# Kernel optimization log

Measured on AMD Instinct MI355X. Metric: run time of the kernel, lower is better.

## Reference

```python
import jax, jax.numpy as jnp
import numpy as np

N_HEADS = 16
DIM_HEAD = 64
ROPE_THETA = 10000.0


def _rope_tables(seq_len, dim_head, dtype):
    # [N, dim_head//2] angle tables, llama-style interleaved-pair rotation
    inv_freq = 1.0 / (ROPE_THETA ** (jnp.arange(0, dim_head, 2, dtype=jnp.float32) / dim_head))
    t = jnp.arange(seq_len, dtype=jnp.float32)
    freqs = jnp.outer(t, inv_freq)  # [N, D/2]
    return jnp.cos(freqs).astype(dtype), jnp.sin(freqs).astype(dtype)


def _apply_rope(x, cos, sin):
    # x: [B, H, N, D]; rotate interleaved pairs (x[2i], x[2i+1])
    xr = x[..., 0::2]
    xi = x[..., 1::2]
    cos = cos[None, None, :, :]
    sin = sin[None, None, :, :]
    out_r = xr * cos - xi * sin
    out_i = xr * sin + xi * cos
    return jnp.stack([out_r, out_i], axis=-1).reshape(x.shape)


def _l2norm(x, eps=1e-12):
    return x / jnp.maximum(jnp.linalg.norm(x, axis=-1, keepdims=True), eps)


def setup_inputs() -> dict:
    key = jax.random.key(0)
    ks = jax.random.split(key, 5)
    B, N, dim = 1, 4096, N_HEADS * DIM_HEAD
    q = jax.random.normal(ks[0], (B, N, dim), dtype=jnp.float32)
    k = jax.random.normal(ks[1], (B, N, dim), dtype=jnp.float32)
    v = jax.random.normal(ks[2], (B, N, dim), dtype=jnp.float32)
    qk_scale = jnp.full((1, 1, 1, DIM_HEAD), 10.0, dtype=jnp.float32)
    w_out = jax.random.normal(ks[3], (dim, dim), dtype=jnp.float32) * (dim ** -0.5)
    b_out = jnp.zeros((dim,), dtype=jnp.float32)
    return {"q": q, "k": k, "v": v, "qk_scale": qk_scale, "w_out": w_out, "b_out": b_out}


def reference(q, k, v, qk_scale, w_out, b_out):
    B, N, dim = q.shape
    H, D = N_HEADS, DIM_HEAD
    scale = D ** -0.5
    # [B, N, dim] -> [B, H, N, D]
    q = q.reshape(B, N, H, D).transpose(0, 2, 1, 3)
    k = k.reshape(B, N, H, D).transpose(0, 2, 1, 3)
    v = v.reshape(B, N, H, D).transpose(0, 2, 1, 3)
    # RoPE
    cos, sin = _rope_tables(N, D, q.dtype)
    q = _apply_rope(q, cos, sin)
    k = _apply_rope(k, cos, sin)
    # QK-norm: L2-normalize then learned scale
    q = _l2norm(q) * qk_scale
    k = _l2norm(k) * qk_scale
    # explicit attention (non-flash)
    scores = jnp.einsum('bhid,bhjd->bhij', q, k) * scale
    probs = jax.nn.softmax(scores, axis=-1)
    out = jnp.einsum('bhij,bhjd->bhid', probs, v)
    out = out.transpose(0, 2, 1, 3).reshape(B, N, dim)
    # Linear: y = x W^T + b
    return out @ w_out.T + b_out
```

## Files before the change

kernel.cpp:

```cpp
#include <hip/hip_runtime.h>
#include <hip/hip_bf16.h>

#define N_CTX 4096
#define NH    16
#define DH    64
#define DIM   1024
#define NSPLIT 4
#define KT_PER_SPLIT (N_CTX / 64 / NSPLIT)

typedef __attribute__((ext_vector_type(8))) short bf16x8;
typedef __attribute__((ext_vector_type(4))) float f32x4;
typedef __attribute__((ext_vector_type(2))) unsigned u32x2;

__device__ __forceinline__ ushort f2bf(float f) {
    union { float f; unsigned u; } x; x.f = f;
    unsigned r = (x.u + 0x7FFFu + ((x.u >> 16) & 1u)) >> 16;
    return (ushort)r;
}
__device__ __forceinline__ float bf2f(ushort u) {
    union { unsigned u; float f; } x; x.u = ((unsigned)u) << 16; return x.f;
}
__device__ __forceinline__ unsigned fbits(float f) {
    union { float f; unsigned u; } x; x.f = f; return x.u;
}
__device__ __forceinline__ unsigned pack_bf16(float lo, float hi) {
    unsigned a = fbits(lo) + 0x8000u;
    unsigned b = fbits(hi) + 0x8000u;
#if defined(__has_builtin)
#if __has_builtin(__builtin_amdgcn_perm)
    return __builtin_amdgcn_perm(b, a, 0x07060302u);
#else
    return (a >> 16) | (b & 0xFFFF0000u);
#endif
#else
    return (a >> 16) | (b & 0xFFFF0000u);
#endif
}
__device__ __forceinline__ float fast_exp2(float x) {
#if defined(__has_builtin)
#if __has_builtin(__builtin_amdgcn_exp2f)
    return __builtin_amdgcn_exp2f(x);
#else
    return exp2f(x);
#endif
#else
    return exp2f(x);
#endif
}
__device__ __forceinline__ void fast_sincos(float ang, float* s, float* c) {
#if defined(__has_builtin)
#if __has_builtin(__builtin_amdgcn_sinf) && __has_builtin(__builtin_amdgcn_cosf) && __has_builtin(__builtin_amdgcn_fractf)
    float rev = __builtin_amdgcn_fractf(ang * 0.15915494309189535f);
    *s = __builtin_amdgcn_sinf(rev);
    *c = __builtin_amdgcn_cosf(rev);
    return;
#endif
#endif
    sincosf(ang, s, c);
}

__device__ __forceinline__ void pl32_swap(unsigned &a, unsigned &b) {
#if defined(__has_builtin)
#if __has_builtin(__builtin_amdgcn_permlane32_swap)
    u32x2 r = __builtin_amdgcn_permlane32_swap(a, b, false, false);
    a = r[0]; b = r[1];
    return;
#endif
#endif
    const int lane = (int)(threadIdx.x & 63);
    unsigned ax = (unsigned)__shfl_xor((int)a, 32, 64);
    unsigned bx = (unsigned)__shfl_xor((int)b, 32, 64);
    unsigned na = (lane & 32) ? bx : a;
    unsigned nb = (lane & 32) ? b  : ax;
    a = na; b = nb;
}
__device__ __forceinline__ void pl16_swap(unsigned &a, unsigned &b) {
#if defined(__has_builtin)
#if __has_builtin(__builtin_amdgcn_permlane16_swap)
    u32x2 r = __builtin_amdgcn_permlane16_swap(a, b, false, false);
    a = r[0]; b = r[1];
    return;
#endif
#endif
    const int lane = (int)(threadIdx.x & 63);
    unsigned ax = (unsigned)__shfl_xor((int)a, 16, 64);
    unsigned bx = (unsigned)__shfl_xor((int)b, 16, 64);
    unsigned na = (lane & 16) ? bx : a;
    unsigned nb = (lane & 16) ? b  : ax;
    a = na; b = nb;
}

#define SC 0.18033688011112042f
#define LF 0.4152410118609203f

__global__ __launch_bounds__(256) void prep_kernel(
    const float* __restrict__ qg, const float* __restrict__ kg,
    const float* __restrict__ qk_scale,
    ushort* __restrict__ qb, ushort* __restrict__ kb)
{
    const int lane = threadIdx.x & 63;
    const int wave = threadIdx.x >> 6;
    const int row  = blockIdx.x * 4 + wave;
    const int n = row >> 4;
    const int h = row & 15;
    const int isk = blockIdx.y;
    const float* __restrict__ x = isk ? kg : qg;
    ushort* __restrict__ xb = isk ? kb : qb;
    const float premul = isk ? 1.0f : SC;

    float val = x[(size_t)n * DIM + h * DH + lane];
    float other = __shfl_xor(val, 1, 64);

    const int i = lane >> 1;
    float inv_freq = fast_exp2((float)i * -LF);
    float ang = (float)n * inv_freq;
    float s, c;
    fast_sincos(ang, &s, &c);

    float r = (lane & 1) ? fmaf(other, s, val * c)
                         : fmaf(val, c, -(other * s));

    float ss = r * r;
    #pragma unroll
    for (int off = 32; off > 0; off >>= 1)
        ss += __shfl_xor(ss, off, 64);
    float invn = rsqrtf(fmaxf(ss, 1e-24f));
    float scl  = qk_scale[lane] * premul;

    xb[((size_t)h * N_CTX + n) * DH + lane] = f2bf(r * invn * scl);
}

__global__ __launch_bounds__(256) void vtrans_kernel(
    const float* __restrict__ v, ushort* __restrict__ vt)
{
    __shared__ ushort L[64][68];
    const int kt = blockIdx.x, h = blockIdx.y, t = threadIdx.x;

    for (int e = t; e < 4096; e += 256) {
        int key = e >> 6, d = e & 63;
        float f = v[(size_t)(kt * 64 + key) * DIM + h * DH + d];
        L[d][key] = f2bf(f);
    }
    __syncthreads();
    for (int e = t; e < 4096; e += 256) {
        int d = e >> 6, key = e & 63;
        vt[((size_t)h * DH + d) * N_CTX + kt * 64 + key] = L[d][key];
    }
}

__global__ __launch_bounds__(256) void wconv_kernel(
    const float* __restrict__ w, ushort* __restrict__ wb)
{
    int i = (blockIdx.x * 256 + threadIdx.x) * 4;
    float4 f = *(const float4*)&w[i];
    ushort4 u;
    u.x = f2bf(f.x); u.y = f2bf(f.y); u.z = f2bf(f.z); u.w = f2bf(f.w);
    *(ushort4*)&wb[i] = u;
}

__global__ __launch_bounds__(256) void attn_kernel(
    const ushort* __restrict__ qb, const ushort* __restrict__ kb,
    const ushort* __restrict__ vt, ushort* __restrict__ opart,
    float* __restrict__ lpart)
{
    __shared__ ushort Ks[64][72];
    __shared__ ushort Vt[64][72];

    const int h     = blockIdx.y;
    const int qbase = blockIdx.x * 128;
    const int sp    = blockIdx.z;
    const int kbase = sp * (N_CTX / NSPLIT);
    const int t    = threadIdx.x;
    const int w    = t >> 6;
    const int lane = t & 63;
    const int l15  = lane & 15;
    const int quad = lane >> 4;

    bf16x8 qf[2][2];
    #pragma unroll
    for (int qt = 0; qt < 2; qt++) {
        const size_t qrow = ((size_t)h * N_CTX + qbase + w * 32 + qt * 16 + l15) * DH;
        qf[qt][0] = *(const bf16x8*)&qb[qrow + quad * 8];
        qf[qt][1] = *(const bf16x8*)&qb[qrow + 32 + quad * 8];
    }

    float l_part[2] = {0.0f, 0.0f};
    f32x4 o_acc[4][2];
    #pragma unroll
    for (int dt = 0; dt < 4; dt++)
        #pragma unroll
        for (int qt = 0; qt < 2; qt++)
            o_acc[dt][qt] = (f32x4){0.f, 0.f, 0.f, 0.f};

    const int sr = t >> 3;
    const int sc = (t & 7) * 8;
    const ushort* kp0 = &kb[((size_t)h * N_CTX + kbase + sr) * DH + sc];
    const ushort* kp1 = kp0 + (size_t)32 * DH;
    const ushort* vp0 = &vt[((size_t)h * DH + sr) * N_CTX + kbase + sc];
    const ushort* vp1 = vp0 + (size_t)32 * N_CTX;
    bf16x8 kr0 = *(const bf16x8*)kp0, kr1 = *(const bf16x8*)kp1;
    bf16x8 vr0 = *(const bf16x8*)vp0, vr1 = *(const bf16x8*)vp1;

    for (int kt = 0; kt < KT_PER_SPLIT; kt++) {
        __syncthreads();
        *(bf16x8*)&Ks[sr][sc]      = kr0;
        *(bf16x8*)&Ks[sr + 32][sc] = kr1;
        *(bf16x8*)&Vt[sr][sc]      = vr0;
        *(bf16x8*)&Vt[sr + 32][sc] = vr1;
        __syncthreads();
        if (kt + 1 < KT_PER_SPLIT) {
            kr0 = *(const bf16x8*)(kp0 + (size_t)(kt + 1) * 64 * DH);
            kr1 = *(const bf16x8*)(kp1 + (size_t)(kt + 1) * 64 * DH);
            vr0 = *(const bf16x8*)(vp0 + (size_t)(kt + 1) * 64);
            vr1 = *(const bf16x8*)(vp1 + (size_t)(kt + 1) * 64);
        }

        #pragma unroll
        for (int jp = 0; jp < 2; jp++) {
            unsigned pa[2][2], pb[2][2];
            #pragma unroll
            for (int jj = 0; jj < 2; jj++) {
                const int j = jp * 2 + jj;
                bf16x8 kf0 = *(const bf16x8*)&Ks[j * 16 + l15][quad * 8];
                bf16x8 kf1 = *(const bf16x8*)&Ks[j * 16 + l15][32 + quad * 8];
                f32x4 s0 = (f32x4){0.f, 0.f, 0.f, 0.f};
                f32x4 s1 = (f32x4){0.f, 0.f, 0.f, 0.f};
                s0 = __builtin_amdgcn_mfma_f32_16x16x32_bf16(kf0, qf[0][0], s0, 0, 0, 0);
                s1 = __builtin_amdgcn_mfma_f32_16x16x32_bf16(kf0, qf[1][0], s1, 0, 0, 0);
                s0 = __builtin_amdgcn_mfma_f32_16x16x32_bf16(kf1, qf[0][1], s0, 0, 0, 0);
                s1 = __builtin_amdgcn_mfma_f32_16x16x32_bf16(kf1, qf[1][1], s1, 0, 0, 0);

                {
                    float p0 = fast_exp2(s0.x), p1 = fast_exp2(s0.y);
                    float p2 = fast_exp2(s0.z), p3 = fast_exp2(s0.w);
                    l_part[0] += (p0 + p1) + (p2 + p3);
                    unsigned d0 = pack_bf16(p0, p1), d1 = pack_bf16(p2, p3);
                    if (jj == 0) { pa[0][0] = d0; pa[0][1] = d1; }
                    else         { pb[0][0] = d0; pb[0][1] = d1; }
                }
                {
                    float p0 = fast_exp2(s1.x), p1 = fast_exp2(s1.y);
                    float p2 = fast_exp2(s1.z), p3 = fast_exp2(s1.w);
                    l_part[1] += (p0 + p1) + (p2 + p3);
                    unsigned d0 = pack_bf16(p0, p1), d1 = pack_bf16(p2, p3);
                    if (jj == 0) { pa[1][0] = d0; pa[1][1] = d1; }
                    else         { pb[1][0] = d0; pb[1][1] = d1; }
                }
            }

            bf16x8 pw[2];
            #pragma unroll
            for (int qt = 0; qt < 2; qt++) {
                unsigned x0 = pa[qt][0], y0 = pb[qt][0];
                unsigned x1 = pa[qt][1], y1 = pb[qt][1];
                pl32_swap(x0, y0);
                pl32_swap(x1, y1);
                pl16_swap(x0, y0);
                pl16_swap(x1, y1);
                uint4 wd; wd.x = x0; wd.y = x1; wd.z = y0; wd.w = y1;
                pw[qt] = __builtin_bit_cast(bf16x8, wd);
            }

            #pragma unroll
            for (int dt = 0; dt < 4; dt++) {
                bf16x8 vf = *(const bf16x8*)&Vt[dt * 16 + l15][jp * 32 + quad * 8];
                o_acc[dt][0] = __builtin_amdgcn_mfma_f32_16x16x32_bf16(vf, pw[0], o_acc[dt][0], 0, 0, 0);
                o_acc[dt][1] = __builtin_amdgcn_mfma_f32_16x16x32_bf16(vf, pw[1], o_acc[dt][1], 0, 0, 0);
            }
        }
    }

    #pragma unroll
    for (int qt = 0; qt < 2; qt++) {
        float v = l_part[qt];
        v += __shfl_xor(v, 16, 64);
        v += __shfl_xor(v, 32, 64);
        if (quad == 0)
            lpart[(size_t)sp * NH * N_CTX + (size_t)h * N_CTX
                  + qbase + w * 32 + qt * 16 + l15] = v;
    }

    #pragma unroll
    for (int qt = 0; qt < 2; qt++)
        #pragma unroll
        for (int dt = 0; dt < 4; dt++) {
            f32x4 o = o_acc[dt][qt];
            ushort4 ov;
            ov.x = f2bf(o.x); ov.y = f2bf(o.y);
            ov.z = f2bf(o.z); ov.w = f2bf(o.w);
            *(ushort4*)&opart[((size_t)sp * N_CTX + qbase + w * 32 + qt * 16 + l15) * DIM
                              + h * DH + dt * 16 + quad * 4] = ov;
        }
}

__global__ __launch_bounds__(256) void combine_kernel(
    const ushort* __restrict__ opart, const float* __restrict__ lpart,
    ushort* __restrict__ attnb)
{
    const int idx = blockIdx.x * 256 + threadIdx.x;
    const int n   = idx >> 8;
    const int rem = idx & 255;
    const int h   = rem >> 4;
    const size_t e = (size_t)n * DIM + h * DH + (rem & 15) * 4;

    float s0 = 0.f, s1 = 0.f, s2 = 0.f, s3 = 0.f, lsum = 0.f;
    #pragma unroll
    for (int sp = 0; sp < NSPLIT; sp++) {
        ushort4 u = *(const ushort4*)&opart[(size_t)sp * N_CTX * DIM + e];
        s0 += bf2f(u.x); s1 += bf2f(u.y); s2 += bf2f(u.z); s3 += bf2f(u.w);
        lsum += lpart[(size_t)sp * NH * N_CTX + (size_t)h * N_CTX + n];
    }
    float li = 1.0f / lsum;

    ushort4 r;
    r.x = f2bf(s0 * li); r.y = f2bf(s1 * li);
    r.z = f2bf(s2 * li); r.w = f2bf(s3 * li);
    *(ushort4*)&attnb[e] = r;
}

__global__ __launch_bounds__(256) void proj_kernel(
    const ushort* __restrict__ A, const ushort* __restrict__ W,
    const float* __restrict__ bias, float* __restrict__ out)
{
    __shared__ ushort As[64][72];
    __shared__ ushort Ws[64][72];

    const int nbase = blockIdx.x * 64;
    const int obase = blockIdx.y * 64;
    const int t    = threadIdx.x;
    const int w    = t >> 6;
    const int lane = t & 63;
    const int l15  = lane & 15;
    const int quad = lane >> 4;
    const int rw   = (w >> 1) * 32;
    const int cw   = (w & 1) * 32;

    f32x4 acc[2][2];
    #pragma unroll
    for (int mt = 0; mt < 2; mt++)
        #pragma unroll
        for (int nt = 0; nt < 2; nt++)
            acc[mt][nt] = (f32x4){0.f, 0.f, 0.f, 0.f};

    for (int kt = 0; kt < DIM / 64; kt++) {
        const int kb = kt * 64;
        __syncthreads();
        #pragma unroll
        for (int i = 0; i < 2; i++) {
            int c = t + i * 256, r = c >> 3, c8 = c & 7;
            *(bf16x8*)&As[r][c8 * 8] =
                *(const bf16x8*)&A[(size_t)(nbase + r) * DIM + kb + c8 * 8];
        }
        #pragma unroll
        for (int i = 0; i < 2; i++) {
            int c = t + i * 256, r = c >> 3, c8 = c & 7;
            *(bf16x8*)&Ws[r][c8 * 8] =
                *(const bf16x8*)&W[(size_t)(obase + r) * DIM + kb + c8 * 8];
        }
        __syncthreads();

        bf16x8 af[2][2], bfr[2][2];
        #pragma unroll
        for (int mt = 0; mt < 2; mt++)
            #pragma unroll
            for (int kh = 0; kh < 2; kh++)
                af[mt][kh] = *(const bf16x8*)&As[rw + mt * 16 + l15][kh * 32 + quad * 8];
        #pragma unroll
        for (int nt = 0; nt < 2; nt++)
            #pragma unroll
            for (int kh = 0; kh < 2; kh++)
                bfr[nt][kh] = *(const bf16x8*)&Ws[cw + nt * 16 + l15][kh * 32 + quad * 8];

        #pragma unroll
        for (int mt = 0; mt < 2; mt++)
            #pragma unroll
            for (int nt = 0; nt < 2; nt++) {
                acc[mt][nt] = __builtin_amdgcn_mfma_f32_16x16x32_bf16(af[mt][0], bfr[nt][0], acc[mt][nt], 0, 0, 0);
                acc[mt][nt] = __builtin_amdgcn_mfma_f32_16x16x32_bf16(af[mt][1], bfr[nt][1], acc[mt][nt], 0, 0, 0);
            }
    }

    #pragma unroll
    for (int nt = 0; nt < 2; nt++) {
        int o = obase + cw + nt * 16 + l15;
        float bb = bias[o];
        #pragma unroll
        for (int mt = 0; mt < 2; mt++) {
            int nrow = nbase + rw + mt * 16 + quad * 4;
            out[(size_t)(nrow + 0) * DIM + o] = acc[mt][nt].x + bb;
            out[(size_t)(nrow + 1) * DIM + o] = acc[mt][nt].y + bb;
            out[(size_t)(nrow + 2) * DIM + o] = acc[mt][nt].z + bb;
            out[(size_t)(nrow + 3) * DIM + o] = acc[mt][nt].w + bb;
        }
    }
}

extern "C" void kernel_launch(void* const* d_in, const int* in_sizes, int n_in,
                              void* d_out, int out_size, void* d_ws, size_t ws_size,
                              hipStream_t stream)
{
    const float* q        = (const float*)d_in[0];
    const float* k        = (const float*)d_in[1];
    const float* v        = (const float*)d_in[2];
    const float* qk_scale = (const float*)d_in[3];
    const float* w_out    = (const float*)d_in[4];
    const float* b_out    = (const float*)d_in[5];
    float* out = (float*)d_out;

    const size_t per = (size_t)NH * N_CTX * DH;
    ushort* qb    = (ushort*)d_ws;
    ushort* kb    = qb + per;
    ushort* vtg   = kb + per;
    ushort* attnb = vtg + per;
    ushort* wb    = attnb + per;
    ushort* opart = wb + (size_t)DIM * DIM;
    float*  lpart = (float*)(opart + (size_t)NSPLIT * N_CTX * DIM);

    prep_kernel<<<dim3(N_CTX * NH / 4, 2), 256, 0, stream>>>(q, k, qk_scale, qb, kb);
    vtrans_kernel<<<dim3(N_CTX / 64, NH), 256, 0, stream>>>(v, vtg);
    wconv_kernel<<<dim3(DIM * DIM / 1024), 256, 0, stream>>>(w_out, wb);
    attn_kernel<<<dim3(N_CTX / 128, NH, NSPLIT), 256, 0, stream>>>(qb, kb, vtg, opart, lpart);
    combine_kernel<<<dim3(N_CTX * DIM / 4 / 256), 256, 0, stream>>>(opart, lpart, attnb);
    proj_kernel<<<dim3(N_CTX / 64, DIM / 64), 256, 0, stream>>>(attnb, wb, b_out, out);
}
```

Measured before the change: 240.0 us.

## Double-buffer LDS tiles in attention and projection kernels with one barrier per step

Both the attention kernel and the output projection GEMM now keep two LDS buffers for the K/V (or A/W) tiles. The next tile is loaded from global memory into registers before the current tile's MFMA work, then written to the other buffer after it, so only one __syncthreads is needed per iteration instead of two. The projection kernel also gains a register prefetch stage it lacked before, letting global loads overlap compute. In exchange, LDS use doubles per block, which can reduce occupancy, and register pressure rises in the projection kernel.

```diff
diff --git a/kernel.cpp b/kernel.cpp
--- a/kernel.cpp
+++ b/kernel.cpp
@@ -163,8 +163,8 @@
     const ushort* __restrict__ vt, ushort* __restrict__ opart,
     float* __restrict__ lpart)
 {
-    __shared__ ushort Ks[64][72];
-    __shared__ ushort Vt[64][72];
+    __shared__ ushort Ks[2][64][72];
+    __shared__ ushort Vt[2][64][72];
 
     const int h     = blockIdx.y;
     const int qbase = blockIdx.x * 128;
@@ -198,21 +198,25 @@
     const ushort* kp1 = kp0 + (size_t)32 * DH;
     const ushort* vp0 = &vt[((size_t)h * DH + sr) * N_CTX + kbase + sc];
     const ushort* vp1 = vp0 + (size_t)32 * N_CTX;
+
     bf16x8 kr0 = *(const bf16x8*)kp0, kr1 = *(const bf16x8*)kp1;
     bf16x8 vr0 = *(const bf16x8*)vp0, vr1 = *(const bf16x8*)vp1;
+    kp0 += (size_t)64 * DH; kp1 += (size_t)64 * DH;
+    vp0 += 64;              vp1 += 64;
+    *(bf16x8*)&Ks[0][sr][sc]      = kr0;
+    *(bf16x8*)&Ks[0][sr + 32][sc] = kr1;
+    *(bf16x8*)&Vt[0][sr][sc]      = vr0;
+    *(bf16x8*)&Vt[0][sr + 32][sc] = vr1;
+    __syncthreads();
 
     for (int kt = 0; kt < KT_PER_SPLIT; kt++) {
-        __syncthreads();
-        *(bf16x8*)&Ks[sr][sc]      = kr0;
-        *(bf16x8*)&Ks[sr + 32][sc] = kr1;
-        *(bf16x8*)&Vt[sr][sc]      = vr0;
-        *(bf16x8*)&Vt[sr + 32][sc] = vr1;
-        __syncthreads();
-        if (kt + 1 < KT_PER_SPLIT) {
-            kr0 = *(const bf16x8*)(kp0 + (size_t)(kt + 1) * 64 * DH);
-            kr1 = *(const bf16x8*)(kp1 + (size_t)(kt + 1) * 64 * DH);
-            vr0 = *(const bf16x8*)(vp0 + (size_t)(kt + 1) * 64);
-            vr1 = *(const bf16x8*)(vp1 + (size_t)(kt + 1) * 64);
+        const int cur = kt & 1;
+        const bool more = (kt + 1 < KT_PER_SPLIT);
+        if (more) {
+            kr0 = *(const bf16x8*)kp0;  kp0 += (size_t)64 * DH;
+            kr1 = *(const bf16x8*)kp1;  kp1 += (size_t)64 * DH;
+            vr0 = *(const bf16x8*)vp0;  vp0 += 64;
+            vr1 = *(const bf16x8*)vp1;  vp1 += 64;
         }
 
         #pragma unroll
@@ -221,8 +225,8 @@
             #pragma unroll
             for (int jj = 0; jj < 2; jj++) {
                 const int j = jp * 2 + jj;
-                bf16x8 kf0 = *(const bf16x8*)&Ks[j * 16 + l15][quad * 8];
-                bf16x8 kf1 = *(const bf16x8*)&Ks[j * 16 + l15][32 + quad * 8];
+                bf16x8 kf0 = *(const bf16x8*)&Ks[cur][j * 16 + l15][quad * 8];
+                bf16x8 kf1 = *(const bf16x8*)&Ks[cur][j * 16 + l15][32 + quad * 8];
                 f32x4 s0 = (f32x4){0.f, 0.f, 0.f, 0.f};
                 f32x4 s1 = (f32x4){0.f, 0.f, 0.f, 0.f};
                 s0 = __builtin_amdgcn_mfma_f32_16x16x32_bf16(kf0, qf[0][0], s0, 0, 0, 0);
@@ -263,10 +267,18 @@
 
             #pragma unroll
             for (int dt = 0; dt < 4; dt++) {
-                bf16x8 vf = *(const bf16x8*)&Vt[dt * 16 + l15][jp * 32 + quad * 8];
+                bf16x8 vf = *(const bf16x8*)&Vt[cur][dt * 16 + l15][jp * 32 + quad * 8];
                 o_acc[dt][0] = __builtin_amdgcn_mfma_f32_16x16x32_bf16(vf, pw[0], o_acc[dt][0], 0, 0, 0);
                 o_acc[dt][1] = __builtin_amdgcn_mfma_f32_16x16x32_bf16(vf, pw[1], o_acc[dt][1], 0, 0, 0);
             }
+        }
+
+        if (more) {
+            *(bf16x8*)&Ks[cur ^ 1][sr][sc]      = kr0;
+            *(bf16x8*)&Ks[cur ^ 1][sr + 32][sc] = kr1;
+            *(bf16x8*)&Vt[cur ^ 1][sr][sc]      = vr0;
+            *(bf16x8*)&Vt[cur ^ 1][sr + 32][sc] = vr1;
+            __syncthreads();
         }
     }
 
@@ -322,8 +334,8 @@
     const ushort* __restrict__ A, const ushort* __restrict__ W,
     const float* __restrict__ bias, float* __restrict__ out)
 {
-    __shared__ ushort As[64][72];
-    __shared__ ushort Ws[64][72];
+    __shared__ ushort As[2][64][72];
+    __shared__ ushort Ws[2][64][72];
 
     const int nbase = blockIdx.x * 64;
     const int obase = blockIdx.y * 64;
@@ -342,34 +354,43 @@
         for (int nt = 0; nt < 2; nt++)
             acc[mt][nt] = (f32x4){0.f, 0.f, 0.f, 0.f};
 
+    const int sr = t >> 3;
+    const int sc = (t & 7) * 8;
+    const ushort* ap0 = &A[(size_t)(nbase + sr) * DIM + sc];
+    const ushort* ap1 = ap0 + (size_t)32 * DIM;
+    const ushort* wp0 = &W[(size_t)(obase + sr) * DIM + sc];
+    const ushort* wp1 = wp0 + (size_t)32 * DIM;
+
+    bf16x8 ar0 = *(const bf16x8*)ap0, ar1 = *(const bf16x8*)ap1;
+    bf16x8 wr0 = *(const bf16x8*)wp0, wr1 = *(const bf16x8*)wp1;
+    ap0 += 64; ap1 += 64; wp0 += 64; wp1 += 64;
+    *(bf16x8*)&As[0][sr][sc]      = ar0;
+    *(bf16x8*)&As[0][sr + 32][sc] = ar1;
+    *(bf16x8*)&Ws[0][sr][sc]      = wr0;
+    *(bf16x8*)&Ws[0][sr + 32][sc] = wr1;
+    __syncthreads();
+
     for (int kt = 0; kt < DIM / 64; kt++) {
-        const int kb = kt * 64;
-        __syncthreads();
-        #pragma unroll
-        for (int i = 0; i < 2; i++) {
-            int c = t + i * 256, r = c >> 3, c8 = c & 7;
-            *(bf16x8*)&As[r][c8 * 8] =
-                *(const bf16x8*)&A[(size_t)(nbase + r) * DIM + kb + c8 * 8];
-        }
-        #pragma unroll
-        for (int i = 0; i < 2; i++) {
-            int c = t + i * 256, r = c >> 3, c8 = c & 7;
-            *(bf16x8*)&Ws[r][c8 * 8] =
-                *(const bf16x8*)&W[(size_t)(obase + r) * DIM + kb + c8 * 8];
-        }
-        __syncthreads();
+        const int cur = kt & 1;
+        const bool more = (kt + 1 < DIM / 64);
+        if (more) {
+            ar0 = *(const bf16x8*)ap0;  ap0 += 64;
+            ar1 = *(const bf16x8*)ap1;  ap1 += 64;
+            wr0 = *(const bf16x8*)wp0;  wp0 += 64;
+            wr1 = *(const bf16x8*)wp1;  wp1 += 64;
+        }
 
         bf16x8 af[2][2], bfr[2][2];
         #pragma unroll
         for (int mt = 0; mt < 2; mt++)
             #pragma unroll
             for (int kh = 0; kh < 2; kh++)
-                af[mt][kh] = *(const bf16x8*)&As[rw + mt * 16 + l15][kh * 32 + quad * 8];
+                af[mt][kh] = *(const bf16x8*)&As[cur][rw + mt * 16 + l15][kh * 32 + quad * 8];
         #pragma unroll
         for (int nt = 0; nt < 2; nt++)
             #pragma unroll
             for (int kh = 0; kh < 2; kh++)
-                bfr[nt][kh] = *(const bf16x8*)&Ws[cw + nt * 16 + l15][kh * 32 + quad * 8];
+                bfr[nt][kh] = *(const bf16x8*)&Ws[cur][cw + nt * 16 + l15][kh * 32 + quad * 8];
 
         #pragma unroll
         for (int mt = 0; mt < 2; mt++)
@@ -378,6 +399,14 @@
                 acc[mt][nt] = __builtin_amdgcn_mfma_f32_16x16x32_bf16(af[mt][0], bfr[nt][0], acc[mt][nt], 0, 0, 0);
                 acc[mt][nt] = __builtin_amdgcn_mfma_f32_16x16x32_bf16(af[mt][1], bfr[nt][1], acc[mt][nt], 0, 0, 0);
             }
+
+        if (more) {
+            *(bf16x8*)&As[cur ^ 1][sr][sc]      = ar0;
+            *(bf16x8*)&As[cur ^ 1][sr + 32][sc] = ar1;
+            *(bf16x8*)&Ws[cur ^ 1][sr][sc]      = wr0;
+            *(bf16x8*)&Ws[cur ^ 1][sr + 32][sc] = wr1;
+            __syncthreads();
+        }
     }
 
     #pragma unroll
```

After: 241.0 us. Within noise of the previous version (+0.4%).
